# Kernel optimization log

Hardware: AMD Instinct MI355X
Metric: run time of the kernel (lower is better)

## Reference

```python
import jax, jax.numpy as jnp
import numpy as np

D_MODEL = 512
NUM_HEADS = 8
D_K = D_MODEL // NUM_HEADS


def setup_inputs() -> dict:
    key = jax.random.key(0)
    ks = jax.random.split(key, 13)
    B, S = 2, 4096
    s = 1.0 / np.sqrt(D_MODEL)
    inp = {
        'Q': jax.random.normal(ks[0], (B, S, D_MODEL), jnp.float32),
        'K': jax.random.normal(ks[1], (B, S, D_MODEL), jnp.float32),
        'V': jax.random.normal(ks[2], (B, S, D_MODEL), jnp.float32),
        'mask': jax.random.randint(ks[3], (B, S), 0, 2, jnp.int32),
        'W_q': jax.random.normal(ks[4], (D_MODEL, D_MODEL), jnp.float32) * s,
        'b_q': jnp.zeros((D_MODEL,), jnp.float32),
        'W_k': jax.random.normal(ks[5], (D_MODEL, D_MODEL), jnp.float32) * s,
        'b_k': jnp.zeros((D_MODEL,), jnp.float32),
        'W_v': jax.random.normal(ks[6], (D_MODEL, D_MODEL), jnp.float32) * s,
        'b_v': jnp.zeros((D_MODEL,), jnp.float32),
        'W_o': jax.random.normal(ks[7], (D_MODEL, D_MODEL), jnp.float32) * s,
        'b_o': jnp.zeros((D_MODEL,), jnp.float32),
    }
    return inp


def _split_heads(x):
    B, S, _ = x.shape
    return x.reshape(B, S, NUM_HEADS, D_K).transpose(0, 2, 1, 3)  # [B,H,S,d_k]


def reference(Q, K, V, mask, W_q, b_q, W_k, b_k, W_v, b_v, W_o, b_o):
    q = _split_heads(Q @ W_q.T + b_q)
    k = _split_heads(K @ W_k.T + b_k)
    v = _split_heads(V @ W_v.T + b_v)
    scores = jnp.einsum('bhqd,bhkd->bhqk', q, k) / jnp.sqrt(jnp.float32(D_K))
    # mask [B,S] broadcast over heads and query dim (key dim masked)
    scores = jnp.where(mask[:, None, None, :] == 0, jnp.float32(-1e9), scores)
    probs = jax.nn.softmax(scores, axis=-1)
    attn = jnp.einsum('bhqk,bhkd->bhqd', probs, v)
    B, H, S, dk = attn.shape
    combined = attn.transpose(0, 2, 1, 3).reshape(B, S, D_MODEL)
    return combined @ W_o.T + b_o
```

## Files before the change

kernel.cpp:

```cpp
#include <hip/hip_runtime.h>
#include <hip/hip_bf16.h>

typedef _Float16 h8 __attribute__((ext_vector_type(8)));
typedef _Float16 h4 __attribute__((ext_vector_type(4)));
typedef _Float16 h2 __attribute__((ext_vector_type(2)));
typedef float f2 __attribute__((ext_vector_type(2)));
typedef float f4 __attribute__((ext_vector_type(4)));
typedef float f16v __attribute__((ext_vector_type(16)));

#define MFMA32(a, b, c) __builtin_amdgcn_mfma_f32_32x32x16_f16(a, b, c, 0, 0, 0)

static constexpr int DM = 512;
static constexpr int SL = 4096;
static constexpr int NH = 8;
static constexpr int DK = 64;
static constexpr int NB = 2;

__device__ __forceinline__ h2 pk2(float a, float b) {
    return __builtin_bit_cast(h2, __builtin_amdgcn_cvt_pkrtz(a, b));
}
__device__ __forceinline__ h8 cvt8(float4 x, float4 y) {
    union { h2 h[4]; h8 v; } u;
    u.h[0] = pk2(x.x, x.y); u.h[1] = pk2(x.z, x.w);
    u.h[2] = pk2(y.x, y.y); u.h[3] = pk2(y.z, y.w);
    return u.v;
}

__global__ __launch_bounds__(256) void proj_qkv_kernel(
    const float* __restrict__ Qin, const float* __restrict__ Kin,
    const float* __restrict__ Vin,
    const float* __restrict__ Wq, const float* __restrict__ Wk,
    const float* __restrict__ Wv,
    const float* __restrict__ bq, const float* __restrict__ bk,
    const float* __restrict__ bv,
    _Float16* __restrict__ qo, _Float16* __restrict__ ko,
    _Float16* __restrict__ vTo)
{
    const int bid = blockIdx.x;
    const int op  = (bid & 7) * 96 + (bid >> 3);
    const int nt    = op & 3;
    const int panel = op >> 2;
    const int which = panel >> 6;
    const int mt    = panel & 63;

    const float* __restrict__ X    = which == 0 ? Qin : (which == 1 ? Kin : Vin);
    const float* __restrict__ W    = which == 0 ? Wq  : (which == 1 ? Wk  : Wv);
    const float* __restrict__ bias = which == 0 ? bq  : (which == 1 ? bk  : bv);

    __shared__ __align__(16) _Float16 As[2][4096];
    __shared__ __align__(16) _Float16 Bs[2][4096];
    __shared__ __align__(16) _Float16 Vtr[64][144];

    const int t   = threadIdx.x;
    const int w   = t >> 6;
    const int l   = t & 63;
    const int l31 = l & 31;
    const int hi  = l >> 5;
    const int mbase = mt * 128;
    const int nbase = nt * 128;
    const int wm = (w >> 1) * 64;
    const int wn = (w & 1) * 64;

    const int id0 = t, id1 = 256 + t;
    const int r0 = id0 >> 2, c0 = id0 & 3;
    const int r1 = id1 >> 2, c1 = id1 & 3;
    const int sl0 = (c0 ^ (r0 & 3)) * 8;
    const int sl1 = (c1 ^ (r1 & 3)) * 8;
    const float* Xp0 = X + (size_t)(mbase + r0) * DM + c0 * 8;
    const float* Xp1 = X + (size_t)(mbase + r1) * DM + c1 * 8;
    const float* Wp0 = W + (size_t)(nbase + r0) * DM + c0 * 8;
    const float* Wp1 = W + (size_t)(nbase + r1) * DM + c1 * 8;

    f16v acc[2][2] = {};

    {
        float4 a00 = *(const float4*)(Xp0), a01 = *(const float4*)(Xp0 + 4);
        float4 a10 = *(const float4*)(Xp1), a11 = *(const float4*)(Xp1 + 4);
        float4 b00 = *(const float4*)(Wp0), b01 = *(const float4*)(Wp0 + 4);
        float4 b10 = *(const float4*)(Wp1), b11 = *(const float4*)(Wp1 + 4);
        *(h8*)&As[0][r0 * 32 + sl0] = cvt8(a00, a01);
        *(h8*)&As[0][r1 * 32 + sl1] = cvt8(a10, a11);
        *(h8*)&Bs[0][r0 * 32 + sl0] = cvt8(b00, b01);
        *(h8*)&Bs[0][r1 * 32 + sl1] = cvt8(b10, b11);
    }
    __syncthreads();

    int cur = 0;
    for (int step = 0; step < 16; ++step) {
        const int kn = (step + 1) * 32;
        float4 a00, a01, a10, a11, b00, b01, b10, b11;
        const bool more = step + 1 < 16;
        if (more) {
            a00 = *(const float4*)(Xp0 + kn); a01 = *(const float4*)(Xp0 + kn + 4);
            a10 = *(const float4*)(Xp1 + kn); a11 = *(const float4*)(Xp1 + kn + 4);
            b00 = *(const float4*)(Wp0 + kn); b01 = *(const float4*)(Wp0 + kn + 4);
            b10 = *(const float4*)(Wp1 + kn); b11 = *(const float4*)(Wp1 + kn + 4);
        }

        const _Float16* Ac = As[cur];
        const _Float16* Bc = Bs[cur];
        h8 af[2][2], bf[2][2];
#pragma unroll
        for (int ti = 0; ti < 2; ++ti)
#pragma unroll
            for (int s = 0; s < 2; ++s)
                af[ti][s] = *(const h8*)&Ac[(wm + ti * 32 + l31) * 32 +
                                            (((2 * s + hi) ^ (l31 & 3)) << 3)];
#pragma unroll
        for (int tj = 0; tj < 2; ++tj)
#pragma unroll
            for (int s = 0; s < 2; ++s)
                bf[tj][s] = *(const h8*)&Bc[(wn + tj * 32 + l31) * 32 +
                                            (((2 * s + hi) ^ (l31 & 3)) << 3)];
        __builtin_amdgcn_s_setprio(1);
#pragma unroll
        for (int ti = 0; ti < 2; ++ti)
#pragma unroll
            for (int tj = 0; tj < 2; ++tj)
#pragma unroll
                for (int s = 0; s < 2; ++s)
                    acc[ti][tj] = MFMA32(af[ti][s], bf[tj][s], acc[ti][tj]);
        __builtin_amdgcn_s_setprio(0);

        if (more) {
            const int nb2 = cur ^ 1;
            *(h8*)&As[nb2][r0 * 32 + sl0] = cvt8(a00, a01);
            *(h8*)&As[nb2][r1 * 32 + sl1] = cvt8(a10, a11);
            *(h8*)&Bs[nb2][r0 * 32 + sl0] = cvt8(b00, b01);
            *(h8*)&Bs[nb2][r1 * 32 + sl1] = cvt8(b10, b11);
        }
        __syncthreads();
        cur ^= 1;
    }

    if (which < 2) {
        _Float16* dst = (which == 0) ? qo : ko;
#pragma unroll
        for (int tj = 0; tj < 2; ++tj) {
            const int n  = nbase + wn + tj * 32 + l31;
            const float bb = bias[n];
            const int hh = n >> 6;
            const int d  = n & 63;
#pragma unroll
            for (int ti = 0; ti < 2; ++ti) {
#pragma unroll
                for (int j = 0; j < 4; ++j) {
#pragma unroll
                    for (int c = 0; c < 4; ++c) {
                        const int m = mbase + wm + ti * 32 + 8 * j + 4 * hi + c;
                        const int bi = m >> 12;
                        const int s  = m & 4095;
                        dst[((size_t)(bi * NH + hh) * SL + s) * DK + d] =
                            (_Float16)(acc[ti][tj][4 * j + c] + bb);
                    }
                }
            }
        }
    } else {
        const int bi = mbase >> 12;
        const int s0 = mbase & 4095;
#pragma unroll
        for (int nh = 0; nh < 2; ++nh) {
            __syncthreads();
            if ((w & 1) == nh) {
#pragma unroll
                for (int tj = 0; tj < 2; ++tj) {
                    const int d = tj * 32 + l31;
                    const float bb = bias[nbase + nh * 64 + d];
#pragma unroll
                    for (int ti = 0; ti < 2; ++ti) {
#pragma unroll
                        for (int j = 0; j < 4; ++j) {
                            h2 x0 = pk2(acc[ti][tj][4 * j] + bb,
                                        acc[ti][tj][4 * j + 1] + bb);
                            h2 x1 = pk2(acc[ti][tj][4 * j + 2] + bb,
                                        acc[ti][tj][4 * j + 3] + bb);
                            h4 val = {x0[0], x0[1], x1[0], x1[1]};
                            *(h4*)&Vtr[d][wm + ti * 32 + 8 * j + 4 * hi] = val;
                        }
                    }
                }
            }
            __syncthreads();
            {
                const int d = t >> 2, part = t & 3;
                const int hh = nt * 2 + nh;
                _Float16* dstv = vTo + ((size_t)(bi * NH + hh) * DK + d) * SL +
                                 s0 + part * 32;
                h8 v0 = *(const h8*)&Vtr[d][part * 32];
                h8 v1 = *(const h8*)&Vtr[d][part * 32 + 8];
                h8 v2 = *(const h8*)&Vtr[d][part * 32 + 16];
                h8 v3 = *(const h8*)&Vtr[d][part * 32 + 24];
                *(h8*)(dstv)      = v0;
                *(h8*)(dstv + 8)  = v1;
                *(h8*)(dstv + 16) = v2;
                *(h8*)(dstv + 24) = v3;
            }
        }
    }
}

static constexpr int KVB  = 128;
static constexpr int NT2  = SL / KVB;
static constexpr int QBLK = 128;

__device__ __forceinline__ void stage_tiles(
    _Float16* Ktb, _Float16* Vtb,
    const _Float16* kbh, const _Float16* vbh, int kb, int t)
{
    const int w = t >> 6, l = t & 63;
    const char* ksrc = (const char*)(kbh + (size_t)kb * DK);
#pragma unroll
    for (int s2 = 0; s2 < 4; ++s2) {
        const int c  = s2 * 256 + w * 64 + l;
        const int kr = c >> 3;
        const int sl = c & 7;
        const int srow = (kr & ~12) | ((kr & 4) << 1) | ((kr & 8) >> 1);
        const int cs = srow * 8 + (sl ^ (kr & 7));
        char* dst = (char*)Ktb + (size_t)(s2 * 256 + w * 64) * 16;
        __builtin_amdgcn_global_load_lds(
            (const __attribute__((address_space(1))) void*)(ksrc + (size_t)cs * 16),
            (__attribute__((address_space(3))) void*)dst, 16, 0, 0);
    }
#pragma unroll
    for (int s2 = 0; s2 < 4; ++s2) {
        const int c   = s2 * 256 + w * 64 + l;
        const int sub = c >> 9;
        const int c2  = c & 511;
        const int d   = c2 >> 3;
        const int sl  = c2 & 7;
        const _Float16* src = vbh + (size_t)d * SL + kb + sub * 64 +
                              (sl ^ (d & 7)) * 8;
        char* dst = (char*)Vtb + (size_t)(s2 * 256 + w * 64) * 16;
        __builtin_amdgcn_global_load_lds(
            (const __attribute__((address_space(1))) void*)src,
            (__attribute__((address_space(3))) void*)dst, 16, 0, 0);
    }
}

__global__ __launch_bounds__(256) void attn_kernel(
    const _Float16* __restrict__ qg, const _Float16* __restrict__ kg,
    const _Float16* __restrict__ vTg, const int* __restrict__ mask,
    _Float16* __restrict__ comb)
{
    const int t   = threadIdx.x;
    const int w   = t >> 6;
    const int l   = t & 63;
    const int l31 = l & 31;
    const int hi  = l >> 5;
    const int r7  = l31 & 7;
    const int hh  = blockIdx.x & 7;
    const int b   = blockIdx.x >> 3;
    const int qt  = blockIdx.y;

    const _Float16* qbh = qg  + (size_t)(b * NH + hh) * SL * DK;
    const _Float16* kbh = kg  + (size_t)(b * NH + hh) * SL * DK;
    const _Float16* vbh = vTg + (size_t)(b * NH + hh) * DK * SL;
    const int* mrow = mask + b * SL;

    __shared__ __align__(16) _Float16 Kt[2][8192];
    __shared__ __align__(16) _Float16 Vt[2][8192];
    __shared__ __align__(16) float bias_tab[SL];

#pragma unroll
    for (int j = 0; j < 4; ++j) {
        int4 v = *(const int4*)&mrow[t * 16 + j * 4];
        f4 bv;
        bv[0] = v.x ? 0.f : -1e38f; bv[1] = v.y ? 0.f : -1e38f;
        bv[2] = v.z ? 0.f : -1e38f; bv[3] = v.w ? 0.f : -1e38f;
        *(f4*)&bias_tab[t * 16 + j * 4] = bv;
    }

    const _Float16 sch = (_Float16)(0.125f * 1.44269504089f);
    const h8 sc8 = {sch, sch, sch, sch, sch, sch, sch, sch};
    h8 qf[4];
    {
        const _Float16* qp = qbh + (size_t)(qt * QBLK + w * 32 + l31) * DK + hi * 8;
#pragma unroll
        for (int st = 0; st < 4; ++st)
            qf[st] = *(const h8*)(qp + st * 16) * sc8;
    }

    const _Float16 oneh = (_Float16)1.0f;
    const h8 ones = {oneh, oneh, oneh, oneh, oneh, oneh, oneh, oneh};

    stage_tiles(Kt[0], Vt[0], kbh, vbh, 0, t);
    __syncthreads();

    f16v ov[2] = {};
    f16v osum  = {};

    int cur = 0;
    for (int kt = 0; kt < NT2; ++kt) {
        const int kb = kt * KVB;
        if (kt + 1 < NT2)
            stage_tiles(Kt[cur ^ 1], Vt[cur ^ 1], kbh, vbh, kb + KVB, t);

#pragma unroll
        for (int kh = 0; kh < 2; ++kh) {
            const _Float16* Kc = Kt[cur] + kh * 4096;
            const _Float16* Vc = Vt[cur] + kh * 4096;
            const int kbb = kb + kh * 64;

            f16v sc[2];
#pragma unroll
            for (int s = 0; s < 2; ++s) {
                union { f2 q[8]; f16v v; } u;
#pragma unroll
                for (int j = 0; j < 4; ++j) {
                    const int base = kbb + s * 32 + ((j >> 1) << 4) +
                                     ((j & 1) << 2) + (hi << 3);
                    u.q[2 * j]     = *(const f2*)&bias_tab[base];
                    u.q[2 * j + 1] = *(const f2*)&bias_tab[base + 2];
                }
                sc[s] = u.v;
            }

            __builtin_amdgcn_s_setprio(1);
#pragma unroll
            for (int s = 0; s < 2; ++s) {
                const int rb = (s * 32 + l31) * 64;
#pragma unroll
                for (int st = 0; st < 4; ++st) {
                    h8 a = *(const h8*)&Kc[rb + (((st * 2 + hi) ^ r7) << 3)];
                    sc[s] = MFMA32(a, qf[st], sc[s]);
                }
            }
            __builtin_amdgcn_s_setprio(0);

#pragma unroll
            for (int s = 0; s < 2; ++s)
#pragma unroll
                for (int r = 0; r < 16; ++r)
                    sc[s][r] = __builtin_amdgcn_exp2f(sc[s][r]);

            __builtin_amdgcn_s_setprio(1);
#pragma unroll
            for (int ks = 0; ks < 4; ++ks) {
                const int s  = ks >> 1;
                const int e0 = (ks & 1) * 8;
                union { h2 h[4]; h8 v; } pf;
#pragma unroll
                for (int u2 = 0; u2 < 4; ++u2)
                    pf.h[u2] = pk2(sc[s][e0 + 2 * u2], sc[s][e0 + 2 * u2 + 1]);
#pragma unroll
                for (int ds = 0; ds < 2; ++ds) {
                    h8 av = *(const h8*)&Vc[(ds * 32 + l31) * 64 +
                                            (((ks * 2 + hi) ^ r7) << 3)];
                    ov[ds] = MFMA32(av, pf.v, ov[ds]);
                }
                osum = MFMA32(ones, pf.v, osum);
            }
            __builtin_amdgcn_s_setprio(0);
        }

        __syncthreads();
        cur ^= 1;
    }

    const float inv = 1.0f / osum[0];

    _Float16* crow = comb + (size_t)(b * SL + qt * QBLK + w * 32 + l31) * DM + hh * DK;
#pragma unroll
    for (int ds = 0; ds < 2; ++ds) {
#pragma unroll
        for (int j = 0; j < 4; ++j) {
            const int d0 = ds * 32 + j * 8 + hi * 4;
            h2 w0 = pk2(ov[ds][4 * j] * inv,     ov[ds][4 * j + 1] * inv);
            h2 w1 = pk2(ov[ds][4 * j + 2] * inv, ov[ds][4 * j + 3] * inv);
            *(h2*)&crow[d0]     = w0;
            *(h2*)&crow[d0 + 2] = w1;
        }
    }
}

__global__ __launch_bounds__(256) void out_proj_kernel(
    const _Float16* __restrict__ comb, const float* __restrict__ Wo,
    const float* __restrict__ bo, float* __restrict__ out)
{
    const int bid = blockIdx.x;
    const int op  = (bid & 7) * 32 + (bid >> 3);
    const int nt  = op & 3;
    const int mt  = op >> 2;

    __shared__ __align__(16) _Float16 As[2][4096];
    __shared__ __align__(16) _Float16 Bs[2][4096];

    const int t   = threadIdx.x;
    const int w   = t >> 6;
    const int l   = t & 63;
    const int l31 = l & 31;
    const int hi  = l >> 5;
    const int mbase = mt * 128;
    const int nbase = nt * 128;
    const int wm = (w >> 1) * 64;
    const int wn = (w & 1) * 64;

    const int id0 = t, id1 = 256 + t;
    const int r0 = id0 >> 2, c0 = id0 & 3;
    const int r1 = id1 >> 2, c1 = id1 & 3;
    const int sl0 = (c0 ^ (r0 & 3)) * 8;
    const int sl1 = (c1 ^ (r1 & 3)) * 8;
    const _Float16* Ap0 = comb + (size_t)(mbase + r0) * DM + (c0 ^ (r0 & 3)) * 8;
    const _Float16* Ap1 = comb + (size_t)(mbase + r1) * DM + (c1 ^ (r1 & 3)) * 8;
    const float* Wp0 = Wo + (size_t)(nbase + r0) * DM + c0 * 8;
    const float* Wp1 = Wo + (size_t)(nbase + r1) * DM + c1 * 8;

    auto stageA = [&](int buf, int kk) {
        char* d0 = (char*)&As[buf][0] + (size_t)id0 * 16;
        char* d1 = (char*)&As[buf][0] + (size_t)id1 * 16;
        __builtin_amdgcn_global_load_lds(
            (const __attribute__((address_space(1))) void*)(Ap0 + kk),
            (__attribute__((address_space(3))) void*)d0, 16, 0, 0);
        __builtin_amdgcn_global_load_lds(
            (const __attribute__((address_space(1))) void*)(Ap1 + kk),
            (__attribute__((address_space(3))) void*)d1, 16, 0, 0);
    };

    f16v acc[2][2] = {};

    stageA(0, 0);
    {
        float4 b00 = *(const float4*)(Wp0), b01 = *(const float4*)(Wp0 + 4);
        float4 b10 = *(const float4*)(Wp1), b11 = *(const float4*)(Wp1 + 4);
        *(h8*)&Bs[0][r0 * 32 + sl0] = cvt8(b00, b01);
        *(h8*)&Bs[0][r1 * 32 + sl1] = cvt8(b10, b11);
    }
    __syncthreads();

    int cur = 0;
    for (int step = 0; step < 16; ++step) {
        const int kn = (step + 1) * 32;
        const bool more = step + 1 < 16;
        float4 b00, b01, b10, b11;
        if (more) {
            stageA(cur ^ 1, kn);
            b00 = *(const float4*)(Wp0 + kn); b01 = *(const float4*)(Wp0 + kn + 4);
            b10 = *(const float4*)(Wp1 + kn); b11 = *(const float4*)(Wp1 + kn + 4);
        }

        const _Float16* Ac = As[cur];
        const _Float16* Bc = Bs[cur];
        h8 af[2][2], bf[2][2];
#pragma unroll
        for (int ti = 0; ti < 2; ++ti)
#pragma unroll
            for (int s = 0; s < 2; ++s)
                af[ti][s] = *(const h8*)&Ac[(wm + ti * 32 + l31) * 32 +
                                            (((2 * s + hi) ^ (l31 & 3)) << 3)];
#pragma unroll
        for (int tj = 0; tj < 2; ++tj)
#pragma unroll
            for (int s = 0; s < 2; ++s)
                bf[tj][s] = *(const h8*)&Bc[(wn + tj * 32 + l31) * 32 +
                                            (((2 * s + hi) ^ (l31 & 3)) << 3)];
        __builtin_amdgcn_s_setprio(1);
#pragma unroll
        for (int ti = 0; ti < 2; ++ti)
#pragma unroll
            for (int tj = 0; tj < 2; ++tj)
#pragma unroll
                for (int s = 0; s < 2; ++s)
                    acc[ti][tj] = MFMA32(af[ti][s], bf[tj][s], acc[ti][tj]);
        __builtin_amdgcn_s_setprio(0);

        if (more) {
            const int nb2 = cur ^ 1;
            *(h8*)&Bs[nb2][r0 * 32 + sl0] = cvt8(b00, b01);
            *(h8*)&Bs[nb2][r1 * 32 + sl1] = cvt8(b10, b11);
        }
        __syncthreads();
        cur ^= 1;
    }

#pragma unroll
    for (int tj = 0; tj < 2; ++tj) {
        const int n = nbase + wn + tj * 32 + l31;
        const float bb = bo[n];
#pragma unroll
        for (int ti = 0; ti < 2; ++ti) {
#pragma unroll
            for (int j = 0; j < 4; ++j) {
#pragma unroll
                for (int c = 0; c < 4; ++c) {
                    const int m = mbase + wm + ti * 32 + 8 * j + 4 * hi + c;
                    out[(size_t)m * DM + n] = acc[ti][tj][4 * j + c] + bb;
                }
            }
        }
    }
}

extern "C" void kernel_launch(void* const* d_in, const int* in_sizes, int n_in,
                              void* d_out, int out_size, void* d_ws, size_t ws_size,
                              hipStream_t stream)
{
    const float* Q    = (const float*)d_in[0];
    const float* K    = (const float*)d_in[1];
    const float* V    = (const float*)d_in[2];
    const int*   mask = (const int*)d_in[3];
    const float* Wq   = (const float*)d_in[4];
    const float* bq   = (const float*)d_in[5];
    const float* Wk   = (const float*)d_in[6];
    const float* bk   = (const float*)d_in[7];
    const float* Wv   = (const float*)d_in[8];
    const float* bv   = (const float*)d_in[9];
    const float* Wo   = (const float*)d_in[10];
    const float* bo   = (const float*)d_in[11];
    float* out = (float*)d_out;

    _Float16* ws = (_Float16*)d_ws;
    const size_t per = (size_t)NB * NH * SL * DK;
    _Float16* q_ws  = ws;
    _Float16* k_ws  = ws + per;
    _Float16* vT_ws = ws + 2 * per;
    _Float16* comb  = ws + 3 * per;

    proj_qkv_kernel<<<dim3(768), 256, 0, stream>>>(
        Q, K, V, Wq, Wk, Wv, bq, bk, bv, q_ws, k_ws, vT_ws);

    attn_kernel<<<dim3(NB * NH, SL / QBLK), 256, 0, stream>>>(
        q_ws, k_ws, vT_ws, mask, comb);

    out_proj_kernel<<<dim3(256), 256, 0, stream>>>(comb, Wo, bo, out);
}
```

Baseline: 144.5 us.

## Split attention over key halves and merge partials in output projection

Adds a split-K dimension to the attention grid so each block processes half the keys. Each block writes an unnormalised fp16 partial output and its row sums, replacing the MFMA ones-vector sum with scalar adds. The output projection loads both partials, adds them and divides by the total sum before the GEMM, and it now uses register loads where it previously used direct-to-LDS loads. The aim is to raise the block count from 512 to 1024 and halve LDS per block for better occupancy on the many CUs. The cost is extra workspace traffic, fp16 partials scaled by 2^-12 (possible precision loss), and more work in the output-projection stage.

```diff
diff --git a/kernel.cpp b/kernel.cpp
--- a/kernel.cpp
+++ b/kernel.cpp
@@ -200,9 +200,10 @@
     }
 }
 
-static constexpr int KVB  = 128;
-static constexpr int NT2  = SL / KVB;
-static constexpr int QBLK = 128;
+static constexpr int QBLK  = 128;
+static constexpr int KSPL  = 2;
+static constexpr int KHALF = SL / KSPL;
+static constexpr int NTS   = KHALF / 64;
 
 __device__ __forceinline__ void stage_tiles(
     _Float16* Ktb, _Float16* Vtb,
@@ -211,27 +212,24 @@
     const int w = t >> 6, l = t & 63;
     const char* ksrc = (const char*)(kbh + (size_t)kb * DK);
 #pragma unroll
-    for (int s2 = 0; s2 < 4; ++s2) {
+    for (int s2 = 0; s2 < 2; ++s2) {
         const int c  = s2 * 256 + w * 64 + l;
         const int kr = c >> 3;
         const int sl = c & 7;
         const int srow = (kr & ~12) | ((kr & 4) << 1) | ((kr & 8) >> 1);
         const int cs = srow * 8 + (sl ^ (kr & 7));
-        char* dst = (char*)Ktb + (size_t)(s2 * 256 + w * 64) * 16;
+        char* dst = (char*)Ktb + (size_t)(s2 * 4096 + w * 1024);
         __builtin_amdgcn_global_load_lds(
             (const __attribute__((address_space(1))) void*)(ksrc + (size_t)cs * 16),
             (__attribute__((address_space(3))) void*)dst, 16, 0, 0);
     }
 #pragma unroll
-    for (int s2 = 0; s2 < 4; ++s2) {
-        const int c   = s2 * 256 + w * 64 + l;
-        const int sub = c >> 9;
-        const int c2  = c & 511;
-        const int d   = c2 >> 3;
-        const int sl  = c2 & 7;
-        const _Float16* src = vbh + (size_t)d * SL + kb + sub * 64 +
-                              (sl ^ (d & 7)) * 8;
-        char* dst = (char*)Vtb + (size_t)(s2 * 256 + w * 64) * 16;
+    for (int s2 = 0; s2 < 2; ++s2) {
+        const int c  = s2 * 256 + w * 64 + l;
+        const int d  = c >> 3;
+        const int cs = (c & 7) ^ (d & 7);
+        const _Float16* src = vbh + (size_t)d * SL + kb + cs * 8;
+        char* dst = (char*)Vtb + (size_t)(s2 * 4096 + w * 1024);
         __builtin_amdgcn_global_load_lds(
             (const __attribute__((address_space(1))) void*)src,
             (__attribute__((address_space(3))) void*)dst, 16, 0, 0);
@@ -241,7 +239,7 @@
 __global__ __launch_bounds__(256) void attn_kernel(
     const _Float16* __restrict__ qg, const _Float16* __restrict__ kg,
     const _Float16* __restrict__ vTg, const int* __restrict__ mask,
-    _Float16* __restrict__ comb)
+    _Float16* __restrict__ o_ws, float* __restrict__ l_ws)
 {
     const int t   = threadIdx.x;
     const int w   = t >> 6;
@@ -252,23 +250,25 @@
     const int hh  = blockIdx.x & 7;
     const int b   = blockIdx.x >> 3;
     const int qt  = blockIdx.y;
+    const int split = blockIdx.z;
+    const int koff  = split * KHALF;
 
     const _Float16* qbh = qg  + (size_t)(b * NH + hh) * SL * DK;
     const _Float16* kbh = kg  + (size_t)(b * NH + hh) * SL * DK;
     const _Float16* vbh = vTg + (size_t)(b * NH + hh) * DK * SL;
     const int* mrow = mask + b * SL;
 
-    __shared__ __align__(16) _Float16 Kt[2][8192];
-    __shared__ __align__(16) _Float16 Vt[2][8192];
-    __shared__ __align__(16) float bias_tab[SL];
-
-#pragma unroll
-    for (int j = 0; j < 4; ++j) {
-        int4 v = *(const int4*)&mrow[t * 16 + j * 4];
+    __shared__ __align__(16) _Float16 Kt[2][4096];
+    __shared__ __align__(16) _Float16 Vt[2][4096];
+    __shared__ __align__(16) float bias_tab[KHALF];
+
+#pragma unroll
+    for (int j = 0; j < 2; ++j) {
+        int4 v = *(const int4*)&mrow[koff + t * 8 + j * 4];
         f4 bv;
         bv[0] = v.x ? 0.f : -1e38f; bv[1] = v.y ? 0.f : -1e38f;
         bv[2] = v.z ? 0.f : -1e38f; bv[3] = v.w ? 0.f : -1e38f;
-        *(f4*)&bias_tab[t * 16 + j * 4] = bv;
+        *(f4*)&bias_tab[t * 8 + j * 4] = bv;
     }
 
     const _Float16 sch = (_Float16)(0.125f * 1.44269504089f);
@@ -281,102 +281,104 @@
             qf[st] = *(const h8*)(qp + st * 16) * sc8;
     }
 
-    const _Float16 oneh = (_Float16)1.0f;
-    const h8 ones = {oneh, oneh, oneh, oneh, oneh, oneh, oneh, oneh};
-
-    stage_tiles(Kt[0], Vt[0], kbh, vbh, 0, t);
+    stage_tiles(Kt[0], Vt[0], kbh, vbh, koff, t);
     __syncthreads();
 
     f16v ov[2] = {};
-    f16v osum  = {};
+    float ls0 = 0.f, ls1 = 0.f;
 
     int cur = 0;
-    for (int kt = 0; kt < NT2; ++kt) {
-        const int kb = kt * KVB;
-        if (kt + 1 < NT2)
-            stage_tiles(Kt[cur ^ 1], Vt[cur ^ 1], kbh, vbh, kb + KVB, t);
-
-#pragma unroll
-        for (int kh = 0; kh < 2; ++kh) {
-            const _Float16* Kc = Kt[cur] + kh * 4096;
-            const _Float16* Vc = Vt[cur] + kh * 4096;
-            const int kbb = kb + kh * 64;
-
-            f16v sc[2];
-#pragma unroll
-            for (int s = 0; s < 2; ++s) {
-                union { f2 q[8]; f16v v; } u;
-#pragma unroll
-                for (int j = 0; j < 4; ++j) {
-                    const int base = kbb + s * 32 + ((j >> 1) << 4) +
-                                     ((j & 1) << 2) + (hi << 3);
-                    u.q[2 * j]     = *(const f2*)&bias_tab[base];
-                    u.q[2 * j + 1] = *(const f2*)&bias_tab[base + 2];
-                }
-                sc[s] = u.v;
-            }
-
-            __builtin_amdgcn_s_setprio(1);
-#pragma unroll
-            for (int s = 0; s < 2; ++s) {
-                const int rb = (s * 32 + l31) * 64;
-#pragma unroll
-                for (int st = 0; st < 4; ++st) {
-                    h8 a = *(const h8*)&Kc[rb + (((st * 2 + hi) ^ r7) << 3)];
-                    sc[s] = MFMA32(a, qf[st], sc[s]);
-                }
-            }
-            __builtin_amdgcn_s_setprio(0);
-
-#pragma unroll
-            for (int s = 0; s < 2; ++s)
-#pragma unroll
-                for (int r = 0; r < 16; ++r)
-                    sc[s][r] = __builtin_amdgcn_exp2f(sc[s][r]);
-
-            __builtin_amdgcn_s_setprio(1);
-#pragma unroll
-            for (int ks = 0; ks < 4; ++ks) {
-                const int s  = ks >> 1;
-                const int e0 = (ks & 1) * 8;
-                union { h2 h[4]; h8 v; } pf;
-#pragma unroll
-                for (int u2 = 0; u2 < 4; ++u2)
-                    pf.h[u2] = pk2(sc[s][e0 + 2 * u2], sc[s][e0 + 2 * u2 + 1]);
-#pragma unroll
-                for (int ds = 0; ds < 2; ++ds) {
-                    h8 av = *(const h8*)&Vc[(ds * 32 + l31) * 64 +
-                                            (((ks * 2 + hi) ^ r7) << 3)];
-                    ov[ds] = MFMA32(av, pf.v, ov[ds]);
-                }
-                osum = MFMA32(ones, pf.v, osum);
-            }
-            __builtin_amdgcn_s_setprio(0);
-        }
+    for (int kt = 0; kt < NTS; ++kt) {
+        const int kb = koff + kt * 64;
+        if (kt + 1 < NTS)
+            stage_tiles(Kt[cur ^ 1], Vt[cur ^ 1], kbh, vbh, kb + 64, t);
+
+        const _Float16* Kc = Kt[cur];
+        const _Float16* Vc = Vt[cur];
+        const int lb = kt * 64;
+
+        f16v sc[2];
+#pragma unroll
+        for (int s = 0; s < 2; ++s) {
+            union { f2 q[8]; f16v v; } u;
+#pragma unroll
+            for (int j = 0; j < 4; ++j) {
+                const int base = lb + s * 32 + ((j >> 1) << 4) +
+                                 ((j & 1) << 2) + (hi << 3);
+                u.q[2 * j]     = *(const f2*)&bias_tab[base];
+                u.q[2 * j + 1] = *(const f2*)&bias_tab[base + 2];
+            }
+            sc[s] = u.v;
+        }
+
+        __builtin_amdgcn_s_setprio(1);
+#pragma unroll
+        for (int s = 0; s < 2; ++s) {
+            const int rb = (s * 32 + l31) * 64;
+#pragma unroll
+            for (int st = 0; st < 4; ++st) {
+                h8 a = *(const h8*)&Kc[rb + (((st * 2 + hi) ^ r7) << 3)];
+                sc[s] = MFMA32(a, qf[st], sc[s]);
+            }
+        }
+        __builtin_amdgcn_s_setprio(0);
+
+#pragma unroll
+        for (int s = 0; s < 2; ++s)
+#pragma unroll
+            for (int r = 0; r < 16; ++r)
+                sc[s][r] = __builtin_amdgcn_exp2f(sc[s][r]);
+#pragma unroll
+        for (int r = 0; r < 16; ++r) { ls0 += sc[0][r]; ls1 += sc[1][r]; }
+
+        __builtin_amdgcn_s_setprio(1);
+#pragma unroll
+        for (int ks = 0; ks < 4; ++ks) {
+            const int s  = ks >> 1;
+            const int e0 = (ks & 1) * 8;
+            union { h2 h[4]; h8 v; } pf;
+#pragma unroll
+            for (int u2 = 0; u2 < 4; ++u2)
+                pf.h[u2] = pk2(sc[s][e0 + 2 * u2], sc[s][e0 + 2 * u2 + 1]);
+#pragma unroll
+            for (int ds = 0; ds < 2; ++ds) {
+                h8 av = *(const h8*)&Vc[(ds * 32 + l31) * 64 +
+                                        (((ks * 2 + hi) ^ r7) << 3)];
+                ov[ds] = MFMA32(av, pf.v, ov[ds]);
+            }
+        }
+        __builtin_amdgcn_s_setprio(0);
 
         __syncthreads();
         cur ^= 1;
     }
 
-    const float inv = 1.0f / osum[0];
-
-    _Float16* crow = comb + (size_t)(b * SL + qt * QBLK + w * 32 + l31) * DM + hh * DK;
+    float lsum = ls0 + ls1;
+    lsum += __shfl_xor(lsum, 32);
+    const int qrow = qt * QBLK + w * 32 + l31;
+    if (hi == 0)
+        l_ws[((size_t)(split * NB + b) * SL + qrow) * NH + hh] = lsum * 0x1p-12f;
+
+    const float osc = 0x1p-12f;
+    _Float16* orow = o_ws + ((size_t)split * NB * SL + (size_t)b * SL + qrow) * DM +
+                     hh * DK;
 #pragma unroll
     for (int ds = 0; ds < 2; ++ds) {
 #pragma unroll
         for (int j = 0; j < 4; ++j) {
             const int d0 = ds * 32 + j * 8 + hi * 4;
-            h2 w0 = pk2(ov[ds][4 * j] * inv,     ov[ds][4 * j + 1] * inv);
-            h2 w1 = pk2(ov[ds][4 * j + 2] * inv, ov[ds][4 * j + 3] * inv);
-            *(h2*)&crow[d0]     = w0;
-            *(h2*)&crow[d0 + 2] = w1;
+            h2 w0 = pk2(ov[ds][4 * j] * osc,     ov[ds][4 * j + 1] * osc);
+            h2 w1 = pk2(ov[ds][4 * j + 2] * osc, ov[ds][4 * j + 3] * osc);
+            h4 val = {w0[0], w0[1], w1[0], w1[1]};
+            *(h4*)&orow[d0] = val;
         }
     }
 }
 
 __global__ __launch_bounds__(256) void out_proj_kernel(
-    const _Float16* __restrict__ comb, const float* __restrict__ Wo,
-    const float* __restrict__ bo, float* __restrict__ out)
+    const _Float16* __restrict__ o_ws, const float* __restrict__ l_ws,
+    const float* __restrict__ Wo, const float* __restrict__ bo,
+    float* __restrict__ out)
 {
     const int bid = blockIdx.x;
     const int op  = (bid & 7) * 32 + (bid >> 3);
@@ -385,6 +387,7 @@
 
     __shared__ __align__(16) _Float16 As[2][4096];
     __shared__ __align__(16) _Float16 Bs[2][4096];
+    __shared__ float Linv[128][8];
 
     const int t   = threadIdx.x;
     const int w   = t >> 6;
@@ -396,33 +399,52 @@
     const int wm = (w >> 1) * 64;
     const int wn = (w & 1) * 64;
 
+    const size_t NSL = (size_t)NB * SL;
+
+#pragma unroll
+    for (int e = 0; e < 4; ++e) {
+        const int idx = t * 4 + e;
+        const int r = idx >> 3, h = idx & 7;
+        const int m = mbase + r;
+        const float l0 = l_ws[((size_t)m) * NH + h];
+        const float l1 = l_ws[(NSL + (size_t)m) * NH + h];
+        Linv[r][h] = 1.0f / (l0 + l1);
+    }
+
     const int id0 = t, id1 = 256 + t;
     const int r0 = id0 >> 2, c0 = id0 & 3;
     const int r1 = id1 >> 2, c1 = id1 & 3;
     const int sl0 = (c0 ^ (r0 & 3)) * 8;
     const int sl1 = (c1 ^ (r1 & 3)) * 8;
-    const _Float16* Ap0 = comb + (size_t)(mbase + r0) * DM + (c0 ^ (r0 & 3)) * 8;
-    const _Float16* Ap1 = comb + (size_t)(mbase + r1) * DM + (c1 ^ (r1 & 3)) * 8;
+    const _Float16* Ap00 = o_ws + (size_t)(mbase + r0) * DM + c0 * 8;
+    const _Float16* Ap01 = Ap00 + NSL * DM;
+    const _Float16* Ap10 = o_ws + (size_t)(mbase + r1) * DM + c1 * 8;
+    const _Float16* Ap11 = Ap10 + NSL * DM;
     const float* Wp0 = Wo + (size_t)(nbase + r0) * DM + c0 * 8;
     const float* Wp1 = Wo + (size_t)(nbase + r1) * DM + c1 * 8;
 
-    auto stageA = [&](int buf, int kk) {
-        char* d0 = (char*)&As[buf][0] + (size_t)id0 * 16;
-        char* d1 = (char*)&As[buf][0] + (size_t)id1 * 16;
-        __builtin_amdgcn_global_load_lds(
-            (const __attribute__((address_space(1))) void*)(Ap0 + kk),
-            (__attribute__((address_space(3))) void*)d0, 16, 0, 0);
-        __builtin_amdgcn_global_load_lds(
-            (const __attribute__((address_space(1))) void*)(Ap1 + kk),
-            (__attribute__((address_space(3))) void*)d1, 16, 0, 0);
+    __syncthreads();
+
+    auto combine8 = [](h8 x, h8 y, float li) -> h8 {
+        union { h2 h[4]; h8 v; } u;
+#pragma unroll
+        for (int e = 0; e < 4; ++e) {
+            float a0 = ((float)x[2 * e]     + (float)y[2 * e])     * li;
+            float a1 = ((float)x[2 * e + 1] + (float)y[2 * e + 1]) * li;
+            u.h[e] = pk2(a0, a1);
+        }
+        return u.v;
     };
 
     f16v acc[2][2] = {};
 
-    stageA(0, 0);
     {
+        h8 a00 = *(const h8*)Ap00, a01 = *(const h8*)Ap01;
+        h8 a10 = *(const h8*)Ap10, a11 = *(const h8*)Ap11;
         float4 b00 = *(const float4*)(Wp0), b01 = *(const float4*)(Wp0 + 4);
         float4 b10 = *(const float4*)(Wp1), b11 = *(const float4*)(Wp1 + 4);
+        *(h8*)&As[0][r0 * 32 + sl0] = combine8(a00, a01, Linv[r0][(c0 * 8) >> 6]);
+        *(h8*)&As[0][r1 * 32 + sl1] = combine8(a10, a11, Linv[r1][(c1 * 8) >> 6]);
         *(h8*)&Bs[0][r0 * 32 + sl0] = cvt8(b00, b01);
         *(h8*)&Bs[0][r1 * 32 + sl1] = cvt8(b10, b11);
     }
@@ -432,11 +454,16 @@
     for (int step = 0; step < 16; ++step) {
         const int kn = (step + 1) * 32;
         const bool more = step + 1 < 16;
+        h8 a00, a01, a10, a11;
         float4 b00, b01, b10, b11;
+        float li0, li1;
         if (more) {
-            stageA(cur ^ 1, kn);
+            a00 = *(const h8*)(Ap00 + kn); a01 = *(const h8*)(Ap01 + kn);
+            a10 = *(const h8*)(Ap10 + kn); a11 = *(const h8*)(Ap11 + kn);
             b00 = *(const float4*)(Wp0 + kn); b01 = *(const float4*)(Wp0 + kn + 4);
             b10 = *(const float4*)(Wp1 + kn); b11 = *(const float4*)(Wp1 + kn + 4);
+            li0 = Linv[r0][((kn + c0 * 8) >> 6) & 7];
+            li1 = Linv[r1][((kn + c1 * 8) >> 6) & 7];
         }
 
         const _Float16* Ac = As[cur];
@@ -466,6 +493,8 @@
 
         if (more) {
             const int nb2 = cur ^ 1;
+            *(h8*)&As[nb2][r0 * 32 + sl0] = combine8(a00, a01, li0);
+            *(h8*)&As[nb2][r1 * 32 + sl1] = combine8(a10, a11, li1);
             *(h8*)&Bs[nb2][r0 * 32 + sl0] = cvt8(b00, b01);
             *(h8*)&Bs[nb2][r1 * 32 + sl1] = cvt8(b10, b11);
         }
@@ -514,13 +543,14 @@
     _Float16* q_ws  = ws;
     _Float16* k_ws  = ws + per;
     _Float16* vT_ws = ws + 2 * per;
-    _Float16* comb  = ws + 3 * per;
+    _Float16* o_ws  = ws + 3 * per;
+    float*    l_ws  = (float*)(ws + 5 * per);
 
     proj_qkv_kernel<<<dim3(768), 256, 0, stream>>>(
         Q, K, V, Wq, Wk, Wv, bq, bk, bv, q_ws, k_ws, vT_ws);
 
-    attn_kernel<<<dim3(NB * NH, SL / QBLK), 256, 0, stream>>>(
-        q_ws, k_ws, vT_ws, mask, comb);
-
-    out_proj_kernel<<<dim3(256), 256, 0, stream>>>(comb, Wo, bo, out);
-}
+    attn_kernel<<<dim3(NB * NH, SL / QBLK, KSPL), 256, 0, stream>>>(
+        q_ws, k_ws, vT_ws, mask, o_ws, l_ws);
+
+    out_proj_kernel<<<dim3(256), 256, 0, stream>>>(o_ws, l_ws, Wo, bo, out);
+}
```

Result: no change. 142.6 us (-1.4%).
